# Optimization experiments

Measured on AMD Instinct MI355X. Metric: run time of the kernel, lower is better.

The kernel has to match this reference:

```python
import jax, jax.numpy as jnp
import numpy as np

B, H, W, C = 8, 64, 64, 256


def setup_inputs() -> dict:
    key = jax.random.key(0)
    kx, kq, kk, kv = jax.random.split(key, 4)
    scale = 1.0 / np.sqrt(C)
    return {
        "x": jax.random.normal(kx, (B, H, W, C), dtype=jnp.float32),
        "Wq": jax.random.normal(kq, (C, C), dtype=jnp.float32) * scale,
        "Wk": jax.random.normal(kk, (C, C), dtype=jnp.float32) * scale,
        "Wv": jax.random.normal(kv, (C, C), dtype=jnp.float32) * scale,
    }


def reference(x, Wq, Wk, Wv):
    b, h, w, c = x.shape
    n = h * w
    xf = x.reshape(b, n, c)  # flatten spatial dims -> [B, N, C]
    # 1x1 convs (no bias) are per-pixel GEMMs
    q = jnp.einsum("bnc,cd->bnd", xf, Wq)
    k = jnp.einsum("bnc,cd->bnd", xf, Wk)
    v = jnp.einsum("bnc,cd->bnd", xf, Wv)
    # full attention over all HW positions (no 1/sqrt(C) scaling in original)
    scores = jnp.einsum("bnd,bmd->bnm", q, k)  # [B, N, N]
    attn = jax.nn.softmax(scores, axis=-1)
    out = jnp.einsum("bnm,bmd->bnd", attn, v)  # [B, N, C]
    out = out.reshape(b, h, w, c)
    return x * out  # elementwise gate with input
```

## Files before the change

### kernel.cpp

```cpp
#include <hip/hip_runtime.h>

#define BB 8
#define NN 4096
#define CC 256

typedef __attribute__((ext_vector_type(8))) short bfx8;
typedef __attribute__((ext_vector_type(4))) unsigned short usx4;
typedef __attribute__((ext_vector_type(4))) float fx4;
typedef _Float16 hfx8 __attribute__((ext_vector_type(8)));

__device__ inline unsigned short f2bf(float f) {
  union { float f; unsigned u; } c; c.f = f;
  unsigned r = c.u + 0x7fffu + ((c.u >> 16) & 1u);
  return (unsigned short)(r >> 16);
}
__device__ inline float bf2f(unsigned short h) {
  union { unsigned u; float f; } c; c.u = ((unsigned)h) << 16;
  return c.f;
}
__device__ inline unsigned short f2h(float f) {
  union { _Float16 h; unsigned short u; } c; c.h = (_Float16)f;
  return c.u;
}
__device__ inline fx4 MFMA(bfx8 a, bfx8 b, fx4 c) {
  return __builtin_amdgcn_mfma_f32_16x16x32_bf16(a, b, c, 0, 0, 0);
}
__device__ inline fx4 MFMAH(hfx8 a, hfx8 b, fx4 c) {
  return __builtin_amdgcn_mfma_f32_16x16x32_f16(a, b, c, 0, 0, 0);
}

__global__ void wconv(const float* __restrict__ Wq, const float* __restrict__ Wk,
                      const float* __restrict__ Wv,
                      unsigned short* __restrict__ Wth, unsigned short* __restrict__ Wtl) {
  int m = blockIdx.y, n = blockIdx.x, k = threadIdx.x;
  const float* W = (m == 0) ? Wq : (m == 1) ? Wk : Wv;
  float v = W[k * CC + n];
  unsigned short h = f2bf(v);
  unsigned short lo = f2bf(v - bf2f(h));
  int o = (m * CC + n) * CC + k;
  Wth[o] = h; Wtl[o] = lo;
}

template <int PASSES>
__global__ __launch_bounds__(256, 2) void proj(
    const float* __restrict__ x,
    const unsigned short* __restrict__ Wth, const unsigned short* __restrict__ Wtl,
    unsigned short* __restrict__ O0, unsigned short* __restrict__ O1) {
  __shared__ char lds[81920];
  const int m = (PASSES == 1) ? 2 : (int)blockIdx.y;
  const int row0 = blockIdx.x * 64;
  const int t = threadIdx.x;
  const int wv = t >> 6, l = t & 63, lg = l >> 4, ll = l & 15;

  fx4 acc[16];
#pragma unroll
  for (int i = 0; i < 16; ++i) acc[i] = (fx4){0.f, 0.f, 0.f, 0.f};

  const unsigned short* Wmh = Wth + m * CC * CC;
  const unsigned short* Wml = Wtl + m * CC * CC;

  for (int kc = 0; kc < 4; ++kc) {
    __syncthreads();
#pragma unroll
    for (int p = 0; p < 4; ++p) {
      int idx = p * 256 + t;
      int r = idx >> 4, c4 = (idx & 15) << 2;
      fx4 v = *(const fx4*)(x + (size_t)(row0 + r) * CC + kc * 64 + c4);
      usx4 hv, lv;
#pragma unroll
      for (int j = 0; j < 4; ++j) {
        unsigned short h = f2bf(v[j]);
        hv[j] = h;
        if (PASSES == 3) lv[j] = f2bf(v[j] - bf2f(h));
      }
      int bo = r * 128 + (((c4 << 1)) ^ ((r & 7) << 4));
      *(usx4*)(lds + bo) = hv;
      if (PASSES == 3) *(usx4*)(lds + 8192 + bo) = lv;
    }
#pragma unroll
    for (int p = 0; p < 8; ++p) {
      int idx = p * 256 + t;
      int n = idx >> 3, c8 = (idx & 7) << 3;
      int go = n * CC + kc * 64 + c8;
      bfx8 hv = *(const bfx8*)(Wmh + go);
      int bo = n * 128 + (((c8 << 1)) ^ ((n & 7) << 4));
      *(bfx8*)(lds + 16384 + bo) = hv;
      if (PASSES == 3) {
        bfx8 lv = *(const bfx8*)(Wml + go);
        *(bfx8*)(lds + 49152 + bo) = lv;
      }
    }
    __syncthreads();
#pragma unroll
    for (int ds = 0; ds < 2; ++ds) {
      int arow = wv * 16 + ll;
      int akb = ds * 64 + lg * 16;
      bfx8 ah = *(bfx8*)(lds + arow * 128 + (akb ^ ((arow & 7) << 4)));
      bfx8 al;
      if (PASSES == 3) al = *(bfx8*)(lds + 8192 + arow * 128 + (akb ^ ((arow & 7) << 4)));
#pragma unroll
      for (int nt = 0; nt < 16; ++nt) {
        int brow = nt * 16 + ll;
        int bo = brow * 128 + (akb ^ ((brow & 7) << 4));
        bfx8 bh = *(bfx8*)(lds + 16384 + bo);
        acc[nt] = MFMA(ah, bh, acc[nt]);
        if (PASSES == 3) {
          bfx8 bl = *(bfx8*)(lds + 49152 + bo);
          acc[nt] = MFMA(ah, bl, acc[nt]);
          acc[nt] = MFMA(al, bh, acc[nt]);
        }
      }
    }
  }
#pragma unroll
  for (int nt = 0; nt < 16; ++nt) {
#pragma unroll
    for (int r = 0; r < 4; ++r) {
      float v = acc[nt][r];
      int grow = row0 + wv * 16 + lg * 4 + r;
      int col = nt * 16 + ll;
      if (PASSES == 1) {
        int b = grow >> 12, nidx = grow & 4095;
        O0[(((size_t)(b * CC + col)) << 12) + nidx] = f2h(v);
      } else {
        size_t o = (size_t)grow * CC + col;
        (m == 0 ? O0 : O1)[o] = f2h(v);
      }
    }
  }
}

__global__ __launch_bounds__(256, 2) void attn(
    const float* __restrict__ x,
    const unsigned short* __restrict__ Qf, const unsigned short* __restrict__ Kf,
    const unsigned short* __restrict__ Vt, float* __restrict__ out) {
  __shared__ char lds[73728];
  const int b = blockIdx.y, q0 = blockIdx.x * 64;
  const int t = threadIdx.x, wv = t >> 6, l = t & 63, lg = l >> 4, ll = l & 15;

  hfx8 qh[8];
  {
    int qrow = q0 + wv * 16 + ll;
    const unsigned short* ph = Qf + ((size_t)(b * NN + qrow)) * CC + lg * 8;
#pragma unroll
    for (int ds = 0; ds < 8; ++ds) qh[ds] = *(const hfx8*)(ph + ds * 32);
  }

  fx4 acc_o[16];
#pragma unroll
  for (int i = 0; i < 16; ++i) acc_o[i] = (fx4){0.f, 0.f, 0.f, 0.f};
  float mrow[4] = {-1e30f, -1e30f, -1e30f, -1e30f};
  float lrow[4] = {0.f, 0.f, 0.f, 0.f};

  const unsigned short* Kb = Kf + (size_t)b * NN * CC;
  const unsigned short* Vtb = Vt + (size_t)b * CC * NN;
  char* plds = lds + 65536 + wv * 2048;

  const int kkey = t >> 5;
  const int kdb  = (t & 31) << 4;
  const int vd   = t >> 3;
  const int vkb  = (t & 7) << 4;

  bfx8 kreg[8], vreg[8];
#pragma unroll
  for (int p = 0; p < 8; ++p) {
    kreg[p] = *(const bfx8*)((const char*)(Kb + (size_t)(p * 8 + kkey) * CC) + kdb);
    vreg[p] = *(const bfx8*)((const char*)(Vtb + (size_t)(p * 32 + vd) * NN) + vkb);
  }

  for (int kt = 0; kt < 64; ++kt) {
    __syncthreads();
#pragma unroll
    for (int p = 0; p < 8; ++p) {
      int key = p * 8 + kkey;
      *(bfx8*)(lds + (kdb >> 7) * 8192 + key * 128 + ((kdb & 127) ^ ((key & 7) << 4))) = kreg[p];
      int d = p * 32 + vd;
      *(bfx8*)(lds + 32768 + d * 128 + (vkb ^ ((d & 7) << 4))) = vreg[p];
    }
    __syncthreads();
    if (kt < 63) {
      const unsigned short* Kn = Kb + (size_t)(kt + 1) * 64 * CC;
      const unsigned short* Vn = Vtb + (kt + 1) * 64;
#pragma unroll
      for (int p = 0; p < 8; ++p) {
        kreg[p] = *(const bfx8*)((const char*)(Kn + (size_t)(p * 8 + kkey) * CC) + kdb);
        vreg[p] = *(const bfx8*)((const char*)(Vn + (size_t)(p * 32 + vd) * NN) + vkb);
      }
    }
    fx4 accs[4];
#pragma unroll
    for (int i = 0; i < 4; ++i) accs[i] = (fx4){0.f, 0.f, 0.f, 0.f};
#pragma unroll
    for (int ds = 0; ds < 8; ++ds) {
      int dc = ds >> 1, dkb = (ds & 1) * 64 + lg * 16;
#pragma unroll
      for (int nt = 0; nt < 4; ++nt) {
        int krow = nt * 16 + ll;
        hfx8 bh = *(hfx8*)(lds + dc * 8192 + krow * 128 + (dkb ^ ((krow & 7) << 4)));
        accs[nt] = MFMAH(qh[ds], bh, accs[nt]);
      }
    }
    float pm[4];
#pragma unroll
    for (int r = 0; r < 4; ++r)
      pm[r] = fmaxf(fmaxf(accs[0][r], accs[1][r]), fmaxf(accs[2][r], accs[3][r]));
#pragma unroll
    for (int s = 1; s < 16; s <<= 1) {
#pragma unroll
      for (int r = 0; r < 4; ++r) pm[r] = fmaxf(pm[r], __shfl_xor(pm[r], s, 64));
    }
    bool upd = false;
#pragma unroll
    for (int r = 0; r < 4; ++r) upd |= (pm[r] > mrow[r] + 8.f);
    if (__any(upd)) {
#pragma unroll
      for (int r = 0; r < 4; ++r) {
        float mn = fmaxf(mrow[r], pm[r]);
        float scl = __expf(mrow[r] - mn);
        mrow[r] = mn;
        lrow[r] *= scl;
#pragma unroll
        for (int i = 0; i < 16; ++i) acc_o[i][r] *= scl;
      }
    }
    float rs[4] = {0.f, 0.f, 0.f, 0.f};
#pragma unroll
    for (int nt = 0; nt < 4; ++nt)
#pragma unroll
      for (int r = 0; r < 4; ++r) {
        float e = __expf(accs[nt][r] - mrow[r]);
        rs[r] += e;
        int prow = lg * 4 + r, pcol = nt * 16 + ll;
        *(unsigned short*)(plds + prow * 128 + (((pcol << 1)) ^ ((prow & 7) << 4))) = f2h(e);
      }
#pragma unroll
    for (int s = 1; s < 16; s <<= 1) {
#pragma unroll
      for (int r = 0; r < 4; ++r) rs[r] += __shfl_xor(rs[r], s, 64);
    }
#pragma unroll
    for (int r = 0; r < 4; ++r) lrow[r] += rs[r];
#pragma unroll
    for (int ks = 0; ks < 2; ++ks) {
      int kbyte = ks * 64 + lg * 16;
      hfx8 pa = *(hfx8*)(plds + ll * 128 + (kbyte ^ ((ll & 7) << 4)));
#pragma unroll
      for (int nt = 0; nt < 16; ++nt) {
        int vrow = nt * 16 + ll;
        hfx8 bv = *(hfx8*)(lds + 32768 + vrow * 128 + (kbyte ^ ((vrow & 7) << 4)));
        acc_o[nt] = MFMAH(pa, bv, acc_o[nt]);
      }
    }
  }
#pragma unroll
  for (int nt = 0; nt < 16; ++nt)
#pragma unroll
    for (int r = 0; r < 4; ++r) {
      int grow = q0 + wv * 16 + lg * 4 + r;
      int col = nt * 16 + ll;
      size_t o = ((size_t)(b * NN + grow)) * CC + col;
      out[o] = x[o] * (acc_o[nt][r] / lrow[r]);
    }
}

extern "C" void kernel_launch(void* const* d_in, const int* in_sizes, int n_in,
                              void* d_out, int out_size, void* d_ws, size_t ws_size,
                              hipStream_t stream) {
  const float* x  = (const float*)d_in[0];
  const float* Wq = (const float*)d_in[1];
  const float* Wk = (const float*)d_in[2];
  const float* Wv = (const float*)d_in[3];
  float* out = (float*)d_out;
  char* ws = (char*)d_ws;
  const size_t T = (size_t)BB * NN * CC * 2;
  unsigned short* Qf  = (unsigned short*)(ws);
  unsigned short* Kf  = (unsigned short*)(ws + T);
  unsigned short* Vt  = (unsigned short*)(ws + 2 * T);
  unsigned short* Wth = (unsigned short*)(ws + 3 * T);
  unsigned short* Wtl = (unsigned short*)(ws + 3 * T + (size_t)3 * CC * CC * 2);
  if (ws_size < 3 * T + (size_t)6 * CC * CC * 2) return;

  hipLaunchKernelGGL(wconv, dim3(256, 3), dim3(256), 0, stream, Wq, Wk, Wv, Wth, Wtl);
  hipLaunchKernelGGL((proj<3>), dim3(512, 2), dim3(256), 0, stream, x, Wth, Wtl, Qf, Kf);
  hipLaunchKernelGGL((proj<1>), dim3(512, 1), dim3(256), 0, stream, x, Wth, Wtl, Vt, Vt);
  hipLaunchKernelGGL(attn, dim3(64, 8), dim3(256), 0, stream, x, Qf, Kf, Vt, out);
}
```

Measured before the change: 366.5 us.

## Process two 16-row query tiles per wave to reuse K/V LDS fragments

Each wave now handles 32 query rows (two 16-row tiles), so every K and V fragment read from LDS feeds two MFMAs. The block covers 128 queries and the grid is halved, which also halves global K/V streaming per query. Occupancy drops to one block per CU, with roughly doubled accumulator registers and larger LDS. s_setprio hints are added around the MFMA phases. The risks are fewer waves to hide latency, possible register spills, and only 256 blocks across the CUs.

```diff
diff --git a/kernel.cpp b/kernel.cpp
--- a/kernel.cpp
+++ b/kernel.cpp
@@ -130,31 +130,74 @@
   }
 }
 
-__global__ __launch_bounds__(256, 2) void attn(
+#define SOFTMAX(sacc, mrow, lrow, acco, pl)                                        \
+  {                                                                                \
+    float pm[4];                                                                   \
+    _Pragma("unroll") for (int r = 0; r < 4; ++r)                                  \
+      pm[r] = fmaxf(fmaxf(sacc[0][r], sacc[1][r]), fmaxf(sacc[2][r], sacc[3][r])); \
+    _Pragma("unroll") for (int s = 1; s < 16; s <<= 1) {                           \
+      _Pragma("unroll") for (int r = 0; r < 4; ++r)                                \
+        pm[r] = fmaxf(pm[r], __shfl_xor(pm[r], s, 64));                            \
+    }                                                                              \
+    bool upd = false;                                                              \
+    _Pragma("unroll") for (int r = 0; r < 4; ++r) upd |= (pm[r] > mrow[r] + 8.f);  \
+    if (__any(upd)) {                                                              \
+      _Pragma("unroll") for (int r = 0; r < 4; ++r) {                              \
+        float mn = fmaxf(mrow[r], pm[r]);                                          \
+        float scl = __expf(mrow[r] - mn);                                          \
+        mrow[r] = mn; lrow[r] *= scl;                                              \
+        _Pragma("unroll") for (int i = 0; i < 16; ++i) acco[i][r] *= scl;          \
+      }                                                                            \
+    }                                                                              \
+    float rs[4] = {0.f, 0.f, 0.f, 0.f};                                            \
+    _Pragma("unroll") for (int nt = 0; nt < 4; ++nt)                               \
+      _Pragma("unroll") for (int r = 0; r < 4; ++r) {                              \
+        float e = __expf(sacc[nt][r] - mrow[r]);                                   \
+        rs[r] += e;                                                                \
+        int prow = lg * 4 + r, pcol = nt * 16 + ll;                                \
+        *(unsigned short*)((pl) + prow * 128 + (((pcol << 1)) ^ ((prow & 7) << 4))) = f2h(e); \
+      }                                                                            \
+    _Pragma("unroll") for (int s = 1; s < 16; s <<= 1) {                           \
+      _Pragma("unroll") for (int r = 0; r < 4; ++r) rs[r] += __shfl_xor(rs[r], s, 64); \
+    }                                                                              \
+    _Pragma("unroll") for (int r = 0; r < 4; ++r) lrow[r] += rs[r];                \
+  }
+
+__global__ __launch_bounds__(256, 1) void attn(
     const float* __restrict__ x,
     const unsigned short* __restrict__ Qf, const unsigned short* __restrict__ Kf,
     const unsigned short* __restrict__ Vt, float* __restrict__ out) {
-  __shared__ char lds[73728];
-  const int b = blockIdx.y, q0 = blockIdx.x * 64;
+  __shared__ char lds[81920];
+  const int b = blockIdx.y, q0 = blockIdx.x * 128;
   const int t = threadIdx.x, wv = t >> 6, l = t & 63, lg = l >> 4, ll = l & 15;
 
-  hfx8 qh[8];
+  hfx8 q0h[8], q1h[8];
   {
-    int qrow = q0 + wv * 16 + ll;
-    const unsigned short* ph = Qf + ((size_t)(b * NN + qrow)) * CC + lg * 8;
-#pragma unroll
-    for (int ds = 0; ds < 8; ++ds) qh[ds] = *(const hfx8*)(ph + ds * 32);
-  }
-
-  fx4 acc_o[16];
-#pragma unroll
-  for (int i = 0; i < 16; ++i) acc_o[i] = (fx4){0.f, 0.f, 0.f, 0.f};
-  float mrow[4] = {-1e30f, -1e30f, -1e30f, -1e30f};
-  float lrow[4] = {0.f, 0.f, 0.f, 0.f};
+    int qrow = q0 + wv * 32 + ll;
+    const unsigned short* p0 = Qf + ((size_t)(b * NN + qrow)) * CC + lg * 8;
+    const unsigned short* p1 = p0 + (size_t)16 * CC;
+#pragma unroll
+    for (int ds = 0; ds < 8; ++ds) {
+      q0h[ds] = *(const hfx8*)(p0 + ds * 32);
+      q1h[ds] = *(const hfx8*)(p1 + ds * 32);
+    }
+  }
+
+  fx4 accA[16], accB[16];
+#pragma unroll
+  for (int i = 0; i < 16; ++i) {
+    accA[i] = (fx4){0.f, 0.f, 0.f, 0.f};
+    accB[i] = (fx4){0.f, 0.f, 0.f, 0.f};
+  }
+  float m0[4] = {-1e30f, -1e30f, -1e30f, -1e30f};
+  float m1[4] = {-1e30f, -1e30f, -1e30f, -1e30f};
+  float l0[4] = {0.f, 0.f, 0.f, 0.f};
+  float l1[4] = {0.f, 0.f, 0.f, 0.f};
 
   const unsigned short* Kb = Kf + (size_t)b * NN * CC;
   const unsigned short* Vtb = Vt + (size_t)b * CC * NN;
-  char* plds = lds + 65536 + wv * 2048;
+  char* pl0 = lds + 65536 + wv * 4096;
+  char* pl1 = pl0 + 2048;
 
   const int kkey = t >> 5;
   const int kdb  = (t & 31) << 4;
@@ -187,9 +230,13 @@
         vreg[p] = *(const bfx8*)((const char*)(Vn + (size_t)(p * 32 + vd) * NN) + vkb);
       }
     }
-    fx4 accs[4];
-#pragma unroll
-    for (int i = 0; i < 4; ++i) accs[i] = (fx4){0.f, 0.f, 0.f, 0.f};
+    fx4 s0[4], s1[4];
+#pragma unroll
+    for (int i = 0; i < 4; ++i) {
+      s0[i] = (fx4){0.f, 0.f, 0.f, 0.f};
+      s1[i] = (fx4){0.f, 0.f, 0.f, 0.f};
+    }
+    __builtin_amdgcn_s_setprio(1);
 #pragma unroll
     for (int ds = 0; ds < 8; ++ds) {
       int dc = ds >> 1, dkb = (ds & 1) * 64 + lg * 16;
@@ -197,69 +244,39 @@
       for (int nt = 0; nt < 4; ++nt) {
         int krow = nt * 16 + ll;
         hfx8 bh = *(hfx8*)(lds + dc * 8192 + krow * 128 + (dkb ^ ((krow & 7) << 4)));
-        accs[nt] = MFMAH(qh[ds], bh, accs[nt]);
-      }
-    }
-    float pm[4];
-#pragma unroll
-    for (int r = 0; r < 4; ++r)
-      pm[r] = fmaxf(fmaxf(accs[0][r], accs[1][r]), fmaxf(accs[2][r], accs[3][r]));
-#pragma unroll
-    for (int s = 1; s < 16; s <<= 1) {
-#pragma unroll
-      for (int r = 0; r < 4; ++r) pm[r] = fmaxf(pm[r], __shfl_xor(pm[r], s, 64));
-    }
-    bool upd = false;
-#pragma unroll
-    for (int r = 0; r < 4; ++r) upd |= (pm[r] > mrow[r] + 8.f);
-    if (__any(upd)) {
-#pragma unroll
-      for (int r = 0; r < 4; ++r) {
-        float mn = fmaxf(mrow[r], pm[r]);
-        float scl = __expf(mrow[r] - mn);
-        mrow[r] = mn;
-        lrow[r] *= scl;
-#pragma unroll
-        for (int i = 0; i < 16; ++i) acc_o[i][r] *= scl;
-      }
-    }
-    float rs[4] = {0.f, 0.f, 0.f, 0.f};
-#pragma unroll
-    for (int nt = 0; nt < 4; ++nt)
-#pragma unroll
-      for (int r = 0; r < 4; ++r) {
-        float e = __expf(accs[nt][r] - mrow[r]);
-        rs[r] += e;
-        int prow = lg * 4 + r, pcol = nt * 16 + ll;
-        *(unsigned short*)(plds + prow * 128 + (((pcol << 1)) ^ ((prow & 7) << 4))) = f2h(e);
-      }
-#pragma unroll
-    for (int s = 1; s < 16; s <<= 1) {
-#pragma unroll
-      for (int r = 0; r < 4; ++r) rs[r] += __shfl_xor(rs[r], s, 64);
-    }
-#pragma unroll
-    for (int r = 0; r < 4; ++r) lrow[r] += rs[r];
+        s0[nt] = MFMAH(q0h[ds], bh, s0[nt]);
+        s1[nt] = MFMAH(q1h[ds], bh, s1[nt]);
+      }
+    }
+    __builtin_amdgcn_s_setprio(0);
+    SOFTMAX(s0, m0, l0, accA, pl0)
+    SOFTMAX(s1, m1, l1, accB, pl1)
+    __builtin_amdgcn_s_setprio(1);
 #pragma unroll
     for (int ks = 0; ks < 2; ++ks) {
       int kbyte = ks * 64 + lg * 16;
-      hfx8 pa = *(hfx8*)(plds + ll * 128 + (kbyte ^ ((ll & 7) << 4)));
+      hfx8 pa0 = *(hfx8*)(pl0 + ll * 128 + (kbyte ^ ((ll & 7) << 4)));
+      hfx8 pa1 = *(hfx8*)(pl1 + ll * 128 + (kbyte ^ ((ll & 7) << 4)));
 #pragma unroll
       for (int nt = 0; nt < 16; ++nt) {
         int vrow = nt * 16 + ll;
         hfx8 bv = *(hfx8*)(lds + 32768 + vrow * 128 + (kbyte ^ ((vrow & 7) << 4)));
-        acc_o[nt] = MFMAH(pa, bv, acc_o[nt]);
-      }
-    }
+        accA[nt] = MFMAH(pa0, bv, accA[nt]);
+        accB[nt] = MFMAH(pa1, bv, accB[nt]);
+      }
+    }
+    __builtin_amdgcn_s_setprio(0);
   }
 #pragma unroll
   for (int nt = 0; nt < 16; ++nt)
 #pragma unroll
     for (int r = 0; r < 4; ++r) {
-      int grow = q0 + wv * 16 + lg * 4 + r;
       int col = nt * 16 + ll;
-      size_t o = ((size_t)(b * NN + grow)) * CC + col;
-      out[o] = x[o] * (acc_o[nt][r] / lrow[r]);
+      int g0 = q0 + wv * 32 + lg * 4 + r;
+      size_t o0 = ((size_t)(b * NN + g0)) * CC + col;
+      out[o0] = x[o0] * (accA[nt][r] / l0[r]);
+      size_t o1 = o0 + (size_t)16 * CC;
+      out[o1] = x[o1] * (accB[nt][r] / l1[r]);
     }
 }
 
@@ -283,5 +300,5 @@
   hipLaunchKernelGGL(wconv, dim3(256, 3), dim3(256), 0, stream, Wq, Wk, Wv, Wth, Wtl);
   hipLaunchKernelGGL((proj<3>), dim3(512, 2), dim3(256), 0, stream, x, Wth, Wtl, Qf, Kf);
   hipLaunchKernelGGL((proj<1>), dim3(512, 1), dim3(256), 0, stream, x, Wth, Wtl, Vt, Vt);
-  hipLaunchKernelGGL(attn, dim3(64, 8), dim3(256), 0, stream, x, Qf, Kf, Vt, out);
-}
+  hipLaunchKernelGGL(attn, dim3(32, 8), dim3(256), 0, stream, x, Qf, Kf, Vt, out);
+}
```

Result: slower. 461.6 us (+25.9%).

## Double-buffer 32-key K/V tiles and compute transposed scores in attention loop

Applied to the files above, without the earlier changes.

The attention loop now walks 32-key tiles through two LDS buffers, so the next tile is staged while the current one is consumed, with one barrier per iteration instead of two. Scores are computed transposed (K as the A operand), so each lane owns a single query row. That makes the max and sum reductions two shuffles each, and the probabilities can be written to LDS as packed 8-byte stores. The change also adds s_setprio around the MFMA sections and replaces the final division with a reciprocal multiply. The cost is twice as many iterations, each with less MFMA work, plus extra shuffles to broadcast the rescale factors back into the accumulator layout.

```diff
diff --git a/kernel.cpp b/kernel.cpp
--- a/kernel.cpp
+++ b/kernel.cpp
@@ -130,11 +130,31 @@
   }
 }
 
+#define LOADKV(K0)                                                            \
+  {                                                                           \
+    const unsigned short* Kn = Kb + (size_t)(K0) * CC;                        \
+    const unsigned short* Vn = Vtb + (K0);                                    \
+    _Pragma("unroll") for (int c = 0; c < 4; ++c) {                           \
+      kreg[c] = *(const bfx8*)(Kn + (t >> 3) * CC + (t & 7) * 32 + c * 8);    \
+      vreg[c] = *(const bfx8*)(Vn + (size_t)t * NN + c * 8);                  \
+    }                                                                         \
+  }
+
+#define STAGE(kn, vn)                                                         \
+  {                                                                           \
+    _Pragma("unroll") for (int c = 0; c < 4; ++c) {                           \
+      int db = (t & 7) * 64 + c * 16;                                         \
+      *(bfx8*)((kn) + (db >> 7) * 4096 + (t >> 3) * 128 +                     \
+               ((db & 127) ^ (((t >> 3) & 7) << 4))) = kreg[c];               \
+      *(bfx8*)((vn) + t * 64 + ((c ^ (t & 3) ^ ((t >> 2) & 3)) << 4)) = vreg[c]; \
+    }                                                                         \
+  }
+
 __global__ __launch_bounds__(256, 2) void attn(
     const float* __restrict__ x,
     const unsigned short* __restrict__ Qf, const unsigned short* __restrict__ Kf,
     const unsigned short* __restrict__ Vt, float* __restrict__ out) {
-  __shared__ char lds[73728];
+  __shared__ char lds[69632];
   const int b = blockIdx.y, q0 = blockIdx.x * 64;
   const int t = threadIdx.x, wv = t >> 6, l = t & 63, lg = l >> 4, ll = l & 15;
 
@@ -149,109 +169,91 @@
   fx4 acc_o[16];
 #pragma unroll
   for (int i = 0; i < 16; ++i) acc_o[i] = (fx4){0.f, 0.f, 0.f, 0.f};
-  float mrow[4] = {-1e30f, -1e30f, -1e30f, -1e30f};
-  float lrow[4] = {0.f, 0.f, 0.f, 0.f};
+  float mrow = -1e30f, lrow = 0.f;
 
   const unsigned short* Kb = Kf + (size_t)b * NN * CC;
   const unsigned short* Vtb = Vt + (size_t)b * CC * NN;
-  char* plds = lds + 65536 + wv * 2048;
-
-  const int kkey = t >> 5;
-  const int kdb  = (t & 31) << 4;
-  const int vd   = t >> 3;
-  const int vkb  = (t & 7) << 4;
-
-  bfx8 kreg[8], vreg[8];
-#pragma unroll
-  for (int p = 0; p < 8; ++p) {
-    kreg[p] = *(const bfx8*)((const char*)(Kb + (size_t)(p * 8 + kkey) * CC) + kdb);
-    vreg[p] = *(const bfx8*)((const char*)(Vtb + (size_t)(p * 32 + vd) * NN) + vkb);
-  }
-
-  for (int kt = 0; kt < 64; ++kt) {
+  char* plds = lds + 65536 + wv * 1024;
+
+  bfx8 kreg[4], vreg[4];
+  LOADKV(0);
+  STAGE(lds, lds + 16384);
+  LOADKV(32);
+  __syncthreads();
+
+  for (int kt = 0; kt < 128; ++kt) {
+    char* kb = lds + (kt & 1) * 32768;
+    char* vb = kb + 16384;
+    if (kt < 127) {
+      char* kn = lds + ((kt & 1) ^ 1) * 32768;
+      STAGE(kn, kn + 16384);
+      if (kt < 126) LOADKV((kt + 2) * 32);
+    }
+    fx4 sT[2];
+    sT[0] = (fx4){0.f, 0.f, 0.f, 0.f};
+    sT[1] = (fx4){0.f, 0.f, 0.f, 0.f};
+    __builtin_amdgcn_s_setprio(1);
+#pragma unroll
+    for (int ds = 0; ds < 8; ++ds) {
+      int db = ds * 64 + lg * 16;
+#pragma unroll
+      for (int nt = 0; nt < 2; ++nt) {
+        int key = nt * 16 + ll;
+        hfx8 af = *(hfx8*)(kb + (db >> 7) * 4096 + key * 128 +
+                           ((db & 127) ^ ((key & 7) << 4)));
+        sT[nt] = MFMAH(af, qh[ds], sT[nt]);
+      }
+    }
+    __builtin_amdgcn_s_setprio(0);
+    float pm = fmaxf(fmaxf(fmaxf(sT[0][0], sT[0][1]), fmaxf(sT[0][2], sT[0][3])),
+                     fmaxf(fmaxf(sT[1][0], sT[1][1]), fmaxf(sT[1][2], sT[1][3])));
+    pm = fmaxf(pm, __shfl_xor(pm, 16, 64));
+    pm = fmaxf(pm, __shfl_xor(pm, 32, 64));
+    if (__any(pm > mrow + 8.f)) {
+      float mn = fmaxf(mrow, pm);
+      float scl = __expf(mrow - mn);
+      mrow = mn; lrow *= scl;
+      float s0 = __shfl(scl, lg * 4 + 0, 64);
+      float s1 = __shfl(scl, lg * 4 + 1, 64);
+      float s2 = __shfl(scl, lg * 4 + 2, 64);
+      float s3 = __shfl(scl, lg * 4 + 3, 64);
+#pragma unroll
+      for (int i = 0; i < 16; ++i) {
+        acc_o[i][0] *= s0; acc_o[i][1] *= s1; acc_o[i][2] *= s2; acc_o[i][3] *= s3;
+      }
+    }
+    float rs = 0.f;
+#pragma unroll
+    for (int nt = 0; nt < 2; ++nt) {
+      float e0 = __expf(sT[nt][0] - mrow);
+      float e1 = __expf(sT[nt][1] - mrow);
+      float e2 = __expf(sT[nt][2] - mrow);
+      float e3 = __expf(sT[nt][3] - mrow);
+      rs += (e0 + e1) + (e2 + e3);
+      uint2 w;
+      w.x = (unsigned)f2h(e0) | ((unsigned)f2h(e1) << 16);
+      w.y = (unsigned)f2h(e2) | ((unsigned)f2h(e3) << 16);
+      *(uint2*)(plds + ll * 64 + nt * 32 + lg * 8) = w;
+    }
+    rs += __shfl_xor(rs, 16, 64);
+    rs += __shfl_xor(rs, 32, 64);
+    lrow += rs;
+    hfx8 pa = *(hfx8*)(plds + ll * 64 + lg * 16);
+    __builtin_amdgcn_s_setprio(1);
+#pragma unroll
+    for (int nt = 0; nt < 16; ++nt) {
+      int d = nt * 16 + ll;
+      hfx8 bv = *(hfx8*)(vb + d * 64 + ((lg ^ (d & 3) ^ ((d >> 2) & 3)) << 4));
+      acc_o[nt] = MFMAH(pa, bv, acc_o[nt]);
+    }
+    __builtin_amdgcn_s_setprio(0);
     __syncthreads();
-#pragma unroll
-    for (int p = 0; p < 8; ++p) {
-      int key = p * 8 + kkey;
-      *(bfx8*)(lds + (kdb >> 7) * 8192 + key * 128 + ((kdb & 127) ^ ((key & 7) << 4))) = kreg[p];
-      int d = p * 32 + vd;
-      *(bfx8*)(lds + 32768 + d * 128 + (vkb ^ ((d & 7) << 4))) = vreg[p];
-    }
-    __syncthreads();
-    if (kt < 63) {
-      const unsigned short* Kn = Kb + (size_t)(kt + 1) * 64 * CC;
-      const unsigned short* Vn = Vtb + (kt + 1) * 64;
-#pragma unroll
-      for (int p = 0; p < 8; ++p) {
-        kreg[p] = *(const bfx8*)((const char*)(Kn + (size_t)(p * 8 + kkey) * CC) + kdb);
-        vreg[p] = *(const bfx8*)((const char*)(Vn + (size_t)(p * 32 + vd) * NN) + vkb);
-      }
-    }
-    fx4 accs[4];
-#pragma unroll
-    for (int i = 0; i < 4; ++i) accs[i] = (fx4){0.f, 0.f, 0.f, 0.f};
-#pragma unroll
-    for (int ds = 0; ds < 8; ++ds) {
-      int dc = ds >> 1, dkb = (ds & 1) * 64 + lg * 16;
-#pragma unroll
-      for (int nt = 0; nt < 4; ++nt) {
-        int krow = nt * 16 + ll;
-        hfx8 bh = *(hfx8*)(lds + dc * 8192 + krow * 128 + (dkb ^ ((krow & 7) << 4)));
-        accs[nt] = MFMAH(qh[ds], bh, accs[nt]);
-      }
-    }
-    float pm[4];
-#pragma unroll
-    for (int r = 0; r < 4; ++r)
-      pm[r] = fmaxf(fmaxf(accs[0][r], accs[1][r]), fmaxf(accs[2][r], accs[3][r]));
-#pragma unroll
-    for (int s = 1; s < 16; s <<= 1) {
-#pragma unroll
-      for (int r = 0; r < 4; ++r) pm[r] = fmaxf(pm[r], __shfl_xor(pm[r], s, 64));
-    }
-    bool upd = false;
-#pragma unroll
-    for (int r = 0; r < 4; ++r) upd |= (pm[r] > mrow[r] + 8.f);
-    if (__any(upd)) {
-#pragma unroll
-      for (int r = 0; r < 4; ++r) {
-        float mn = fmaxf(mrow[r], pm[r]);
-        float scl = __expf(mrow[r] - mn);
-        mrow[r] = mn;
-        lrow[r] *= scl;
-#pragma unroll
-        for (int i = 0; i < 16; ++i) acc_o[i][r] *= scl;
-      }
-    }
-    float rs[4] = {0.f, 0.f, 0.f, 0.f};
-#pragma unroll
-    for (int nt = 0; nt < 4; ++nt)
-#pragma unroll
-      for (int r = 0; r < 4; ++r) {
-        float e = __expf(accs[nt][r] - mrow[r]);
-        rs[r] += e;
-        int prow = lg * 4 + r, pcol = nt * 16 + ll;
-        *(unsigned short*)(plds + prow * 128 + (((pcol << 1)) ^ ((prow & 7) << 4))) = f2h(e);
-      }
-#pragma unroll
-    for (int s = 1; s < 16; s <<= 1) {
-#pragma unroll
-      for (int r = 0; r < 4; ++r) rs[r] += __shfl_xor(rs[r], s, 64);
-    }
-#pragma unroll
-    for (int r = 0; r < 4; ++r) lrow[r] += rs[r];
-#pragma unroll
-    for (int ks = 0; ks < 2; ++ks) {
-      int kbyte = ks * 64 + lg * 16;
-      hfx8 pa = *(hfx8*)(plds + ll * 128 + (kbyte ^ ((ll & 7) << 4)));
-#pragma unroll
-      for (int nt = 0; nt < 16; ++nt) {
-        int vrow = nt * 16 + ll;
-        hfx8 bv = *(hfx8*)(lds + 32768 + vrow * 128 + (kbyte ^ ((vrow & 7) << 4)));
-        acc_o[nt] = MFMAH(pa, bv, acc_o[nt]);
-      }
-    }
-  }
+  }
+  float l0 = __shfl(lrow, lg * 4 + 0, 64);
+  float l1 = __shfl(lrow, lg * 4 + 1, 64);
+  float l2 = __shfl(lrow, lg * 4 + 2, 64);
+  float l3 = __shfl(lrow, lg * 4 + 3, 64);
+  fx4 linv = (fx4){1.f / l0, 1.f / l1, 1.f / l2, 1.f / l3};
 #pragma unroll
   for (int nt = 0; nt < 16; ++nt)
 #pragma unroll
@@ -259,7 +261,7 @@
       int grow = q0 + wv * 16 + lg * 4 + r;
       int col = nt * 16 + ll;
       size_t o = ((size_t)(b * NN + grow)) * CC + col;
-      out[o] = x[o] * (acc_o[nt][r] / lrow[r]);
+      out[o] = x[o] * (acc_o[nt][r] * linv[r]);
     }
 }
 
```

Measured after the change: 403.4 us. 1.1x slower.
